# Optimization experiments

Hardware: AMD Instinct MI355X
Metric: run time of the kernel (lower is better)

Reference implementation:

```python
import jax, jax.numpy as jnp
import numpy as np

N_DST = 100_000
N_SRC = 200_000
DEG = 16            # fixed avg degree -> E = N_DST*DEG
E = N_DST * DEG
P, K, W = 16, 256, 8  # num_parts, codebook entries, part width; feat_dim = P*W = 128
F_IN = P * W
F_OUT = 128


def setup_inputs() -> dict:
    key = jax.random.key(0)
    k1, k2, k3, k4, k5, k6, k7 = jax.random.split(key, 7)
    codes = jax.random.randint(k1, (N_SRC, P), 0, K, dtype=jnp.int32)
    indices = jax.random.randint(k2, (E,), 0, N_SRC, dtype=jnp.int32)
    indptr = (jnp.arange(N_DST + 1, dtype=jnp.int32) * DEG)
    h_self = jax.random.normal(k3, (N_DST, F_IN), dtype=jnp.float32)
    codebook = jax.random.normal(k4, (P, K, W), dtype=jnp.float32)
    W_neigh = jax.random.normal(k5, (F_OUT, F_IN), dtype=jnp.float32) * (1.0 / np.sqrt(F_IN))
    W_self = jax.random.normal(k6, (F_OUT, F_IN), dtype=jnp.float32) * (1.0 / np.sqrt(F_IN))
    b_self = jax.random.normal(k7, (F_OUT,), dtype=jnp.float32) * 0.01
    return {"codes": codes, "indices": indices, "indptr": indptr, "h_self": h_self,
            "codebook": codebook, "W_neigh": W_neigh, "W_self": W_self, "b_self": b_self}


def reference(codes, indices, indptr, h_self, codebook, W_neigh, W_self, b_self):
    n_dst = indptr.shape[0] - 1
    n_edges = indices.shape[0]
    # --- VQ decompress: codebook[p, codes[n, p]] -> [N_src, P, W] -> [N_src, F_IN]
    feat = codebook[jnp.arange(P)[None, :], codes]          # [N_src, P, W]
    feat = feat.reshape(feat.shape[0], F_IN)                # [N_src, F_IN]
    # --- CSR(CSC) mean SpMM over neighbors
    # dst id of each edge from indptr (jit-safe, static E)
    dst_ids = jnp.searchsorted(indptr, jnp.arange(n_edges, dtype=indptr.dtype), side="right") - 1
    gathered = feat[indices]                                 # [E, F_IN] (irregular gather)
    summed = jax.ops.segment_sum(gathered, dst_ids, num_segments=n_dst)  # [N_dst, F_IN]
    deg = jnp.diff(indptr).astype(summed.dtype)
    h_neigh = summed / jnp.maximum(deg, 1.0)[:, None]        # mean aggregation
    # --- linear combine: fc_neigh(h_neigh) + fc_self(h_self)
    rst = h_neigh @ W_neigh.T + h_self @ W_self.T + b_self[None, :]
    return rst
```

## Files before the change

kernel.cpp:

```cpp
#include <hip/hip_runtime.h>
#include <stdint.h>

constexpr int N_DST = 100000;
constexpr int N_SRC = 200000;
constexpr int DEG   = 16;
constexpr int PP    = 16;
constexpr int KK    = 256;
constexpr int WW    = 8;
constexpr int F_IN  = 128;
constexpr int F_OUT = 128;

typedef __attribute__((ext_vector_type(8))) short short8;
typedef __attribute__((ext_vector_type(4))) float floatx4;

__device__ __forceinline__ unsigned short f2bf(float f) {
    unsigned int u = __float_as_uint(f);
    unsigned int r = (u + 0x7FFFu + ((u >> 16) & 1u)) >> 16;
    return (unsigned short)r;
}
__device__ __forceinline__ float bf2f(unsigned int bits16) {
    return __uint_as_float(bits16 << 16);
}

constexpr int DT = 64;
constexpr int NT = (N_DST + DT - 1) / DT;
constexpr int LDS_STRIDE = 264;

__global__ __launch_bounds__(1024, 4) void fused_kernel(
    const int* __restrict__ codes, const int* __restrict__ indices,
    const float* __restrict__ codebook, const float* __restrict__ h_self,
    const float* __restrict__ Wn, const float* __restrict__ Ws,
    const float* __restrict__ b_self, float* __restrict__ out)
{
    __shared__ __align__(16) unsigned short scb[PP * KK * WW];
    __shared__ __align__(16) unsigned short hcat[2][DT][LDS_STRIDE];

    const int tid  = threadIdx.x;
    const int wv   = tid >> 6;
    const int lane = tid & 63;
    const int quad = lane >> 4;
    const int r    = lane & 15;
    const int p    = lane & 15;
    const int sub  = lane >> 4;

    {
        const float4* cb4 = (const float4*)codebook;
        ushort4* s4 = (ushort4*)scb;
        #pragma unroll
        for (int it = 0; it < 8; ++it) {
            const int i = tid + it * 1024;
            const float4 v = cb4[i];
            ushort4 w;
            w.x = f2bf(v.x); w.y = f2bf(v.y); w.z = f2bf(v.z); w.w = f2bf(v.w);
            s4[i] = w;
        }
    }

    const int cg = wv & 7;
    const int rg = wv >> 3;
    short8 bfrag[8];
    #pragma unroll
    for (int kt = 0; kt < 8; ++kt) {
        const int o  = cg * 16 + r;
        const int kb = kt * 32 + quad * 8;
        const float* src = (kb < 128) ? (Wn + o * 128 + kb)
                                      : (Ws + o * 128 + (kb - 128));
        union { short8 v; unsigned short u[8]; } f;
        #pragma unroll
        for (int j = 0; j < 8; ++j) f.u[j] = f2bf(src[j]);
        bfrag[kt] = f.v;
    }
    const float bs = b_self[cg * 16 + r];

    __syncthreads();

    const int G = gridDim.x;
    int t = blockIdx.x;

    int sidx_cur = 0;
    {
        const int db = t * DT + wv * 4;
        if (db + sub < N_DST) sidx_cur = indices[db * DEG + lane];
    }
    int sidx_nxt = 0;
    if (t + G < NT) {
        const int db = (t + G) * DT + wv * 4;
        if (db + sub < N_DST) sidx_nxt = indices[db * DEG + lane];
    }
    int c_cur[16];
    #pragma unroll
    for (int e = 0; e < 16; ++e) {
        const int s = __shfl(sidx_cur, (lane & 48) | e, 64);
        c_cur[e] = codes[s * PP + p];
    }

    int buf = 0;
    for (; t < NT; t += G) {
        const int d0 = t * DT;

        int sidx_nn = 0;
        if (t + 2 * G < NT) {
            const int db = (t + 2 * G) * DT + wv * 4;
            if (db + sub < N_DST) sidx_nn = indices[db * DEG + lane];
        }

        int c_nxt[16];
        if (t + G < NT) {
            #pragma unroll
            for (int e = 0; e < 16; ++e) {
                const int s = __shfl(sidx_nxt, (lane & 48) | e, 64);
                c_nxt[e] = codes[s * PP + p];
            }
        } else {
            #pragma unroll
            for (int e = 0; e < 16; ++e) c_nxt[e] = 0;
        }

        const int hrow = tid >> 4;
        const int hcol = tid & 15;
        const int hd   = d0 + hrow;
        float4 ha = make_float4(0.f, 0.f, 0.f, 0.f);
        float4 hb = ha;
        if (hd < N_DST) {
            const float4* s4 = (const float4*)(h_self + (size_t)hd * F_IN + hcol * 8);
            ha = s4[0]; hb = s4[1];
        }

        float ga[8];
        #pragma unroll
        for (int i = 0; i < 8; ++i) ga[i] = 0.f;
        #pragma unroll
        for (int e = 0; e < 16; ++e) {
            const uint4 q = *(const uint4*)(scb + (((p << 8) | c_cur[e]) << 3));
            ga[0] += bf2f(q.x & 0xFFFFu);
            ga[1] += bf2f(q.x >> 16);
            ga[2] += bf2f(q.y & 0xFFFFu);
            ga[3] += bf2f(q.y >> 16);
            ga[4] += bf2f(q.z & 0xFFFFu);
            ga[5] += bf2f(q.z >> 16);
            ga[6] += bf2f(q.w & 0xFFFFu);
            ga[7] += bf2f(q.w >> 16);
        }

        {
            uint4 o4;
            o4.x = (unsigned int)f2bf(ga[0] * 0.0625f) | ((unsigned int)f2bf(ga[1] * 0.0625f) << 16);
            o4.y = (unsigned int)f2bf(ga[2] * 0.0625f) | ((unsigned int)f2bf(ga[3] * 0.0625f) << 16);
            o4.z = (unsigned int)f2bf(ga[4] * 0.0625f) | ((unsigned int)f2bf(ga[5] * 0.0625f) << 16);
            o4.w = (unsigned int)f2bf(ga[6] * 0.0625f) | ((unsigned int)f2bf(ga[7] * 0.0625f) << 16);
            *(uint4*)&hcat[buf][wv * 4 + sub][p * 8] = o4;
        }

        {
            uint4 hw;
            hw.x = (unsigned int)f2bf(ha.x) | ((unsigned int)f2bf(ha.y) << 16);
            hw.y = (unsigned int)f2bf(ha.z) | ((unsigned int)f2bf(ha.w) << 16);
            hw.z = (unsigned int)f2bf(hb.x) | ((unsigned int)f2bf(hb.y) << 16);
            hw.w = (unsigned int)f2bf(hb.z) | ((unsigned int)f2bf(hb.w) << 16);
            *(uint4*)&hcat[buf][hrow][128 + hcol * 8] = hw;
        }

        __syncthreads();

        floatx4 acc0 = (floatx4)(0.f);
        floatx4 acc1 = (floatx4)(0.f);
        #pragma unroll
        for (int kt = 0; kt < 8; ++kt) {
            const short8 a0 = *(const short8*)&hcat[buf][rg * 32 + r][kt * 32 + quad * 8];
            const short8 a1 = *(const short8*)&hcat[buf][rg * 32 + 16 + r][kt * 32 + quad * 8];
            acc0 = __builtin_amdgcn_mfma_f32_16x16x32_bf16(a0, bfrag[kt], acc0, 0, 0, 0);
            acc1 = __builtin_amdgcn_mfma_f32_16x16x32_bf16(a1, bfrag[kt], acc1, 0, 0, 0);
        }

        #pragma unroll
        for (int e = 0; e < 4; ++e) {
            const int d = d0 + rg * 32 + quad * 4 + e;
            if (d < N_DST) out[(size_t)d * F_OUT + cg * 16 + r] = acc0[e] + bs;
        }
        #pragma unroll
        for (int e = 0; e < 4; ++e) {
            const int d = d0 + rg * 32 + 16 + quad * 4 + e;
            if (d < N_DST) out[(size_t)d * F_OUT + cg * 16 + r] = acc1[e] + bs;
        }

        #pragma unroll
        for (int e = 0; e < 16; ++e) c_cur[e] = c_nxt[e];
        sidx_nxt = sidx_nn;
        buf ^= 1;
    }
}

extern "C" void kernel_launch(void* const* d_in, const int* in_sizes, int n_in,
                              void* d_out, int out_size, void* d_ws, size_t ws_size,
                              hipStream_t stream) {
    const int*   codes    = (const int*)d_in[0];
    const int*   indices  = (const int*)d_in[1];
    const float* h_self   = (const float*)d_in[3];
    const float* codebook = (const float*)d_in[4];
    const float* W_neigh  = (const float*)d_in[5];
    const float* W_self   = (const float*)d_in[6];
    const float* b_self   = (const float*)d_in[7];
    float*       out      = (float*)d_out;

    fused_kernel<<<256, 1024, 0, stream>>>(codes, indices, codebook, h_self,
                                           W_neigh, W_self, b_self, out);
}
```

Baseline: 165.9 us.

## Transpose LDS codebook layout and drop cross-iteration code prefetch

Stores the bf16 codebook in LDS as [k][p][w] instead of [p][k][w] and indexes it accordingly. Removes the two-stage software prefetch of edge indices and codes, loading them within each tile iteration instead. Relaxes the launch bound's minimum blocks per CU to 1, loosening register constraints. This simplifies register pressure but exposes global gather latency that the prefetch previously hid.

```diff
diff --git a/kernel.cpp b/kernel.cpp
--- a/kernel.cpp
+++ b/kernel.cpp
@@ -26,13 +26,13 @@
 constexpr int NT = (N_DST + DT - 1) / DT;
 constexpr int LDS_STRIDE = 264;
 
-__global__ __launch_bounds__(1024, 4) void fused_kernel(
+__global__ __launch_bounds__(1024, 1) void fused_kernel(
     const int* __restrict__ codes, const int* __restrict__ indices,
     const float* __restrict__ codebook, const float* __restrict__ h_self,
     const float* __restrict__ Wn, const float* __restrict__ Ws,
     const float* __restrict__ b_self, float* __restrict__ out)
 {
-    __shared__ __align__(16) unsigned short scb[PP * KK * WW];
+    __shared__ __align__(16) unsigned short scb[KK * PP * WW];
     __shared__ __align__(16) unsigned short hcat[2][DT][LDS_STRIDE];
 
     const int tid  = threadIdx.x;
@@ -50,9 +50,12 @@
         for (int it = 0; it < 8; ++it) {
             const int i = tid + it * 1024;
             const float4 v = cb4[i];
+            const int pp   = i >> 9;
+            const int k    = (i >> 1) & 255;
+            const int half = i & 1;
             ushort4 w;
             w.x = f2bf(v.x); w.y = f2bf(v.y); w.z = f2bf(v.z); w.w = f2bf(v.w);
-            s4[i] = w;
+            s4[((k << 4) | pp) * 2 + half] = w;
         }
     }
 
@@ -75,46 +78,13 @@
     __syncthreads();
 
     const int G = gridDim.x;
-    int t = blockIdx.x;
-
-    int sidx_cur = 0;
-    {
-        const int db = t * DT + wv * 4;
-        if (db + sub < N_DST) sidx_cur = indices[db * DEG + lane];
-    }
-    int sidx_nxt = 0;
-    if (t + G < NT) {
-        const int db = (t + G) * DT + wv * 4;
-        if (db + sub < N_DST) sidx_nxt = indices[db * DEG + lane];
-    }
-    int c_cur[16];
-    #pragma unroll
-    for (int e = 0; e < 16; ++e) {
-        const int s = __shfl(sidx_cur, (lane & 48) | e, 64);
-        c_cur[e] = codes[s * PP + p];
-    }
-
     int buf = 0;
-    for (; t < NT; t += G) {
+    for (int t = blockIdx.x; t < NT; t += G) {
         const int d0 = t * DT;
 
-        int sidx_nn = 0;
-        if (t + 2 * G < NT) {
-            const int db = (t + 2 * G) * DT + wv * 4;
-            if (db + sub < N_DST) sidx_nn = indices[db * DEG + lane];
-        }
-
-        int c_nxt[16];
-        if (t + G < NT) {
-            #pragma unroll
-            for (int e = 0; e < 16; ++e) {
-                const int s = __shfl(sidx_nxt, (lane & 48) | e, 64);
-                c_nxt[e] = codes[s * PP + p];
-            }
-        } else {
-            #pragma unroll
-            for (int e = 0; e < 16; ++e) c_nxt[e] = 0;
-        }
+        const int dbase = d0 + wv * 4;
+        int sidx = 0;
+        if (dbase + sub < N_DST) sidx = indices[dbase * DEG + lane];
 
         const int hrow = tid >> 4;
         const int hcol = tid & 15;
@@ -126,12 +96,19 @@
             ha = s4[0]; hb = s4[1];
         }
 
+        int c[16];
+        #pragma unroll
+        for (int e = 0; e < 16; ++e) {
+            const int s = __shfl(sidx, (lane & 48) | e, 64);
+            c[e] = codes[s * PP + p];
+        }
+
         float ga[8];
         #pragma unroll
         for (int i = 0; i < 8; ++i) ga[i] = 0.f;
         #pragma unroll
         for (int e = 0; e < 16; ++e) {
-            const uint4 q = *(const uint4*)(scb + (((p << 8) | c_cur[e]) << 3));
+            const uint4 q = *(const uint4*)(scb + (((c[e] << 4) | p) << 3));
             ga[0] += bf2f(q.x & 0xFFFFu);
             ga[1] += bf2f(q.x >> 16);
             ga[2] += bf2f(q.y & 0xFFFFu);
@@ -183,9 +160,6 @@
             if (d < N_DST) out[(size_t)d * F_OUT + cg * 16 + r] = acc1[e] + bs;
         }
 
-        #pragma unroll
-        for (int e = 0; e < 16; ++e) c_cur[e] = c_nxt[e];
-        sidx_nxt = sidx_nn;
         buf ^= 1;
     }
 }
```

After: 161.4 us. 1.03x faster.
